# Performance work log

Hardware: AMD Instinct MI355X
Metric: run time of the kernel (lower is better)

Reference implementation:

```python
import jax, jax.numpy as jnp
import numpy as np

EPS = 1e-5

def conv(x, w, groups=1):
    # x: NCHW, w: OIHW, VALID padding, stride 1 (cross-correlation, same as torch conv2d)
    return jax.lax.conv_general_dilated(x, w, (1, 1), 'VALID',
                                        feature_group_count=groups,
                                        dimension_numbers=('NCHW', 'OIHW', 'NCHW'))

def bn(x, g, b, m, v):
    # eval-mode batchnorm with running stats
    scale = (g / jnp.sqrt(v + EPS))[None, :, None, None]
    return (x - m[None, :, None, None]) * scale + b[None, :, None, None]

def xcorr_depthwise(x, k):
    # x: [B,C,Hs,Ws] search, k: [B,C,Hk,Wk] per-sample kernels
    B, C, H, W = x.shape
    xr = x.reshape(1, B * C, H, W)
    kr = k.reshape(B * C, 1, k.shape[2], k.shape[3])
    out = conv(xr, kr, groups=B * C)  # [1, B*C, Ho, Wo]
    return out.reshape(B, C, out.shape[2], out.shape[3])

def setup_inputs() -> dict:
    key = jax.random.key(0)
    ks = jax.random.split(key, 16)
    Cin, Hid, Cout = 256, 256, 20
    inp = {
        'kernel': jax.random.normal(ks[0], (128, Cin, 7, 7), jnp.float32),
        'search': jax.random.normal(ks[1], (128, Cin, 31, 31), jnp.float32),
        'wk': jax.random.normal(ks[2], (Hid, Cin, 3, 3), jnp.float32) * 0.02,
        'gk': jnp.ones((Hid,), jnp.float32),
        'bk': jnp.zeros((Hid,), jnp.float32),
        'mk': jax.random.normal(ks[3], (Hid,), jnp.float32) * 0.1,
        'vk': jax.random.uniform(ks[4], (Hid,), jnp.float32) + 0.5,
        'ws': jax.random.normal(ks[5], (Hid, Cin, 3, 3), jnp.float32) * 0.02,
        'gs': jnp.ones((Hid,), jnp.float32),
        'bs': jnp.zeros((Hid,), jnp.float32),
        'ms': jax.random.normal(ks[6], (Hid,), jnp.float32) * 0.1,
        'vs': jax.random.uniform(ks[7], (Hid,), jnp.float32) + 0.5,
        'wh1': jax.random.normal(ks[8], (Hid, Hid, 1, 1), jnp.float32) * 0.02,
        'gh': jnp.ones((Hid,), jnp.float32),
        'bh': jnp.zeros((Hid,), jnp.float32),
        'mh': jax.random.normal(ks[9], (Hid,), jnp.float32) * 0.1,
        'vh': jax.random.uniform(ks[10], (Hid,), jnp.float32) + 0.5,
        'wh2': jax.random.normal(ks[11], (Cout, Hid, 1, 1), jnp.float32) * 0.02,
        'bh2': jnp.zeros((Cout,), jnp.float32),
    }
    return inp

def reference(kernel, search, wk, gk, bk, mk, vk, ws, gs, bs, ms, vs,
              wh1, gh, bh, mh, vh, wh2, bh2):
    k = jax.nn.relu(bn(conv(kernel, wk), gk, bk, mk, vk))   # [B,256,5,5]
    s = jax.nn.relu(bn(conv(search, ws), gs, bs, ms, vs))   # [B,256,29,29]
    f = xcorr_depthwise(s, k)                               # [B,256,25,25]
    h = jax.nn.relu(bn(conv(f, wh1), gh, bh, mh, vh))
    out = conv(h, wh2) + bh2[None, :, None, None]           # [B,20,25,25]
    return out
```

## Files before the change

kernel.cpp:

```cpp
#include <hip/hip_runtime.h>

typedef __bf16 bf16x8 __attribute__((ext_vector_type(8)));
typedef float floatx4 __attribute__((ext_vector_type(4)));
typedef unsigned short u16;
typedef unsigned int u32;

__device__ __forceinline__ u16 f2bf(float f) {
    union { float f; unsigned int u; } q; q.f = f;
    unsigned int r = q.u + 0x7FFFu + ((q.u >> 16) & 1u);
    return (u16)(r >> 16);
}
__device__ __forceinline__ float bf2f(u16 b) {
    union { unsigned int u; float f; } q; q.u = ((unsigned int)b) << 16;
    return q.f;
}

__device__ __forceinline__ void gl2lds16(const u16* g, u16* l) {
    __builtin_amdgcn_global_load_lds((const __attribute__((address_space(1))) u32*)g,
                                     (__attribute__((address_space(3))) u32*)l, 16, 0, 0);
}

__global__ __launch_bounds__(256) void prep_and_transpose(
    const float* __restrict__ kin, u16* __restrict__ KIN,
    const float* __restrict__ sin_, u16* __restrict__ SIN,
    const float* __restrict__ wk, const float* __restrict__ wsw, const float* __restrict__ wh1,
    const float* __restrict__ gk, const float* __restrict__ bk,
    const float* __restrict__ mk, const float* __restrict__ vk,
    const float* __restrict__ gs, const float* __restrict__ bs,
    const float* __restrict__ ms, const float* __restrict__ vs,
    const float* __restrict__ gh, const float* __restrict__ bh,
    const float* __restrict__ mh, const float* __restrict__ vh,
    u16* __restrict__ WKP, u16* __restrict__ WSP, u16* __restrict__ WH1P,
    float* __restrict__ par)
{
    __shared__ float tile[64][33];
    int bid = blockIdx.x, t = threadIdx.x;
    if (bid < 16896) {
        const float* in; u16* out; int HW, sptiles;
        if (bid < 1024) { in = kin;  out = KIN; HW = 49;  sptiles = 2; }
        else { bid -= 1024; in = sin_; out = SIN; HW = 961; sptiles = 31; }
        int st  = bid % sptiles;
        int tmp = bid / sptiles;
        int ct  = tmp & 3;
        int b   = tmp >> 2;
        int sp0 = st * 32, ci0 = ct * 64;
        int j = t & 31, i8 = t >> 5;
        const float* ip = in + ((size_t)b * 256 + ci0 + i8) * HW + sp0 + j;
#pragma unroll
        for (int k = 0; k < 8; ++k) {
            if (sp0 + j < HW) tile[i8 + k * 8][j] = ip[(size_t)(k * 8) * HW];
        }
        __syncthreads();
        int cl = t & 63, s4 = t >> 6;
#pragma unroll
        for (int k = 0; k < 8; ++k) {
            int spl = s4 + k * 4;
            int sp  = sp0 + spl;
            if (sp < HW) out[((size_t)b * HW + sp) * 256 + ci0 + cl] = f2bf(tile[cl][spl]);
        }
        return;
    }
    bid -= 16896;
    if (bid < 4608) {
        const float* src = (bid < 2304) ? wk : wsw;
        u16* dst = (bid < 2304) ? WKP : WSP;
        int tid = ((bid < 2304) ? bid : bid - 2304) * 256 + t;
        int o  = tid / 2304;
        int k  = tid - o * 2304;
        int rc = k >> 8;
        int ci = k & 255;
        dst[tid] = f2bf(src[o * 2304 + ci * 9 + rc]);
    } else if (bid < 4864) {
        int tid = (bid - 4608) * 256 + t;
        WH1P[tid] = f2bf(wh1[tid]);
    } else {
        float s;
        s = gk[t] * rsqrtf(vk[t] + 1e-5f); par[0*256+t] = s; par[1*256+t] = bk[t] - mk[t]*s;
        s = gs[t] * rsqrtf(vs[t] + 1e-5f); par[2*256+t] = s; par[3*256+t] = bs[t] - ms[t]*s;
        s = gh[t] * rsqrtf(vh[t] + 1e-5f); par[4*256+t] = s; par[5*256+t] = bh[t] - mh[t]*s;
    }
}

__global__ __launch_bounds__(256) void conv_gemm(
    const u16* __restrict__ Ain, const u16* __restrict__ Wpk,
    const float* __restrict__ scale, const float* __restrict__ shift,
    u16* __restrict__ Out,
    int OHW, int OW, int IW, int bstride, int KW, int nrc, int mblocks)
{
    __shared__ u16 Alds[4096];
    __shared__ u16 Blds[4096];

    const int tot = mblocks * 2;
    const int grp = (tot >> 3) << 3;
    const int lid = blockIdx.x;
    const int nid = (lid < grp) ? ((lid & 7) * (grp >> 3) + (lid >> 3)) : lid;
    const int m0 = (nid >> 1) * 128;
    const int n0 = (nid & 1) * 128;

    const int t    = threadIdx.x;
    const int wave = t >> 6;
    const int lane = t & 63;
    const int quad = lane >> 4;
    const int lrow = lane & 15;

    const int koff = (((t & 3) ^ ((t >> 3) & 3)) << 3);
    const int r0 = t >> 2;
    int m_a0 = m0 + r0;
    int b0 = m_a0 / OHW; int rem0 = m_a0 - b0 * OHW; int y0 = rem0 / OW; int x0 = rem0 - y0 * OW;
    int m_a1 = m_a0 + 64;
    int b1 = m_a1 / OHW; int rem1 = m_a1 - b1 * OHW; int y1 = rem1 / OW; int x1 = rem1 - y1 * OW;
    const u16* ag0 = Ain + (size_t)b0 * bstride + (size_t)(y0 * IW + x0) * 256 + koff;
    const u16* ag1 = Ain + (size_t)b1 * bstride + (size_t)(y1 * IW + x1) * 256 + koff;
    const int Ktot = nrc * 256;
    const u16* bg0 = Wpk + (size_t)(n0 + r0) * Ktot + koff;
    const u16* bg1 = bg0 + (size_t)64 * Ktot;

    u16* lA0 = Alds + wave * 512;
    u16* lA1 = Alds + 2048 + wave * 512;
    u16* lB0 = Blds + wave * 512;
    u16* lB1 = Blds + 2048 + wave * 512;

    floatx4 zero = {0.f, 0.f, 0.f, 0.f};
    floatx4 acc[4][4];
#pragma unroll
    for (int i = 0; i < 4; ++i)
#pragma unroll
        for (int j = 0; j < 4; ++j) acc[i][j] = zero;

    const int wr  = (wave >> 1) << 6;
    const int wc  = (wave & 1) << 6;
    const int pos = ((quad ^ ((lrow >> 1) & 3)) << 3);

    const int nchunks = nrc << 3;
    for (int ch = 0; ch < nchunks; ++ch) {
        int rc  = ch >> 3;
        int ci0 = (ch & 7) << 5;
        int rr  = rc / KW;
        int cc  = rc - rr * KW;
        int ao  = (rr * IW + cc) * 256 + ci0;
        int bo  = ch << 5;
        __syncthreads();
        gl2lds16(ag0 + ao, lA0);
        gl2lds16(ag1 + ao, lA1);
        gl2lds16(bg0 + bo, lB0);
        gl2lds16(bg1 + bo, lB1);
        __syncthreads();
        bf16x8 af[4], bfr[4];
#pragma unroll
        for (int mi = 0; mi < 4; ++mi)
            af[mi] = *(const bf16x8*)&Alds[(wr + mi * 16 + lrow) * 32 + pos];
#pragma unroll
        for (int ni = 0; ni < 4; ++ni)
            bfr[ni] = *(const bf16x8*)&Blds[(wc + ni * 16 + lrow) * 32 + pos];
#pragma unroll
        for (int mi = 0; mi < 4; ++mi)
#pragma unroll
            for (int ni = 0; ni < 4; ++ni)
                acc[mi][ni] = __builtin_amdgcn_mfma_f32_16x16x32_bf16(af[mi], bfr[ni], acc[mi][ni], 0, 0, 0);
    }

    float sc[4], sh[4];
#pragma unroll
    for (int ni = 0; ni < 4; ++ni) {
        int gn = n0 + wc + ni * 16 + lrow;
        sc[ni] = scale[gn];
        sh[ni] = shift[gn];
    }
#pragma unroll
    for (int mi = 0; mi < 4; ++mi) {
        int gm = m0 + wr + mi * 16 + (quad << 2);
#pragma unroll
        for (int ri = 0; ri < 4; ++ri) {
            size_t ro = (size_t)(gm + ri) * 256 + n0 + wc + lrow;
#pragma unroll
            for (int ni = 0; ni < 4; ++ni) {
                float v = acc[mi][ni][ri] * sc[ni] + sh[ni];
                v = fmaxf(v, 0.f);
                Out[ro + ni * 16] = f2bf(v);
            }
        }
    }
}

#define NS_BLK 421
__global__ __launch_bounds__(512, 2) void conv_gemm256(
    const u16* __restrict__ AinS, const u16* __restrict__ WpkS,
    const float* __restrict__ parS, u16* __restrict__ OutS,
    const u16* __restrict__ AinK, const u16* __restrict__ WpkK,
    const float* __restrict__ parK, u16* __restrict__ OutK)
{
    __shared__ __align__(16) u16 Alds[2][256][64];
    __shared__ __align__(16) u16 Blds[2][256][64];

    const int Ktot = 2304;
    const int NKT  = 36;
    const int KW   = 3;

    const int lid = blockIdx.x;
    const bool isk = (lid >= NS_BLK);

    int nid;
    if (!isk) {
        const int xcd = lid & 7, sub = lid >> 3;
        nid = (xcd < 5) ? (xcd * 53 + sub) : (265 + (xcd - 5) * 52 + sub);
    } else {
        nid = lid - NS_BLK;
    }
    const int m0 = nid << 8;

    const int OHW     = isk ? 25    : 841;
    const int OW      = isk ? 5     : 29;
    const int IW      = isk ? 7     : 31;
    const int bstride = isk ? 12544 : 246016;
    const int Mtot    = isk ? 3200  : 107648;
    const u16* Ain    = isk ? AinK : AinS;
    const u16* Wpk    = isk ? WpkK : WpkS;
    const float* scale = isk ? parK : parS;
    const float* shift = scale + 256;
    u16* Out          = isk ? OutK : OutS;

    const int t     = threadIdx.x;
    const int wave  = t >> 6;
    const int lane  = t & 63;
    const int lrow  = lane & 15;
    const int lquad = lane >> 4;
    const int wmBase = (wave >> 2) << 7;
    const int wnBase = (wave & 3) << 6;

    const u16* pA[4];
    const u16* pB[4];
#pragma unroll
    for (int j = 0; j < 4; ++j) {
        int u = j * 512 + t;
        int row = u >> 3, slot = u & 7;
        int ko = ((slot ^ (row & 7)) << 3);
        int m = m0 + row; if (m >= Mtot) m = Mtot - 1;
        int b = m / OHW; int rem = m - b * OHW; int y = rem / OW; int x = rem - y * OW;
        pA[j] = Ain + (size_t)b * bstride + (size_t)(y * IW + x) * 256 + ko;
        pB[j] = Wpk + (size_t)row * (size_t)Ktot + ko;
    }

    const int xo0 = ((lquad ^ (lrow & 7)) << 3);
    const int xo1 = xo0 ^ 32;

    floatx4 acc[8][4];
#pragma unroll
    for (int i = 0; i < 8; ++i)
#pragma unroll
        for (int j = 0; j < 4; ++j) acc[i][j] = (floatx4){0.f, 0.f, 0.f, 0.f};

#pragma unroll
    for (int j = 0; j < 4; ++j)
        gl2lds16(pA[j], &Alds[0][0][0] + j * 4096 + wave * 512);
#pragma unroll
    for (int j = 0; j < 4; ++j)
        gl2lds16(pB[j], &Blds[0][0][0] + j * 4096 + wave * 512);
    asm volatile("s_waitcnt vmcnt(0)" ::: "memory");
    __builtin_amdgcn_s_barrier();

#define LOADA(mb) do {                                              \
        const u16* _p = Ab + (wmBase + (mb) * 16 + lrow) * 64;      \
        aF[0][0] = *(const bf16x8*)(_p + xo0);                      \
        aF[0][1] = *(const bf16x8*)(_p + xo1);                      \
        aF[1][0] = *(const bf16x8*)(_p + 1024 + xo0);               \
        aF[1][1] = *(const bf16x8*)(_p + 1024 + xo1);               \
    } while (0)

#define MFMA16(mb) do {                                                                               \
        _Pragma("unroll")                                                                             \
        for (int _n = 0; _n < 4; ++_n) {                                                              \
            acc[(mb)][_n]     = __builtin_amdgcn_mfma_f32_16x16x32_bf16(aF[0][0], bB[_n][0], acc[(mb)][_n], 0, 0, 0);     \
            acc[(mb)][_n]     = __builtin_amdgcn_mfma_f32_16x16x32_bf16(aF[0][1], bB[_n][1], acc[(mb)][_n], 0, 0, 0);     \
            acc[(mb) + 1][_n] = __builtin_amdgcn_mfma_f32_16x16x32_bf16(aF[1][0], bB[_n][0], acc[(mb) + 1][_n], 0, 0, 0); \
            acc[(mb) + 1][_n] = __builtin_amdgcn_mfma_f32_16x16x32_bf16(aF[1][1], bB[_n][1], acc[(mb) + 1][_n], 0, 0, 0); \
        }                                                                                             \
    } while (0)

#pragma unroll 2
    for (int kt = 0; kt < NKT; ++kt) {
        const int c = kt & 1;
        const u16* Ab = &Alds[c][0][0];
        const u16* Bb = &Blds[c][0][0];
        u16* An = &Alds[c ^ 1][0][0];
        u16* Bn = &Blds[c ^ 1][0][0];
        const int pf = (kt + 1 < NKT);
        const int kt1 = kt + 1;
        const int rc = kt1 >> 2;
        const int rr = rc / KW;
        const int cc = rc - rr * KW;
        const int aoffA = (rr * IW + cc) * 256 + ((kt1 & 3) << 6);
        const int boffB = kt1 << 6;

        if (pf) {
#pragma unroll
            for (int j = 0; j < 4; ++j)
                gl2lds16(pA[j] + aoffA, An + j * 4096 + wave * 512);
#pragma unroll
            for (int j = 0; j < 4; ++j)
                gl2lds16(pB[j] + boffB, Bn + j * 4096 + wave * 512);
        }

        bf16x8 bB[4][2];
        bf16x8 aF[2][2];
#pragma unroll
        for (int ni = 0; ni < 4; ++ni) {
            const u16* _p = Bb + (wnBase + ni * 16 + lrow) * 64;
            bB[ni][0] = *(const bf16x8*)(_p + xo0);
            bB[ni][1] = *(const bf16x8*)(_p + xo1);
        }
        LOADA(0);
        MFMA16(0);
        LOADA(2);
        MFMA16(2);
        LOADA(4);
        MFMA16(4);
        LOADA(6);
        MFMA16(6);

        asm volatile("s_waitcnt vmcnt(0)" ::: "memory");
        __builtin_amdgcn_s_barrier();
    }

#undef LOADA
#undef MFMA16

    float sc[4], sh[4];
#pragma unroll
    for (int ni = 0; ni < 4; ++ni) {
        int gn = wnBase + ni * 16 + lrow;
        sc[ni] = scale[gn];
        sh[ni] = shift[gn];
    }
#pragma unroll
    for (int mi = 0; mi < 8; ++mi) {
        int gm0 = m0 + wmBase + mi * 16 + (lquad << 2);
#pragma unroll
        for (int ri = 0; ri < 4; ++ri) {
            int gm = gm0 + ri;
            if (gm < Mtot) {
                size_t ro = (size_t)gm * 256 + wnBase + lrow;
#pragma unroll
                for (int ni = 0; ni < 4; ++ni) {
                    float v = acc[mi][ni][ri] * sc[ni] + sh[ni];
                    v = fmaxf(v, 0.f);
                    Out[ro + ni * 16] = f2bf(v);
                }
            }
        }
    }
}

__global__ __launch_bounds__(256) void xcorr(const u16* __restrict__ ss, const u16* __restrict__ kk,
                                             u16* __restrict__ f) {
    __shared__ __align__(16) u16 Srow[29 * 256];

    int lid = blockIdx.x;
    int bid = (lid & 7) * 400 + (lid >> 3);
    int b = bid / 25, y = bid - b * 25;
    int t = threadIdx.x;
    int cg = (t & 31) << 3;
    int xg = t >> 5;
    const u16* kbase = kk + (size_t)b * 25 * 256 + cg;
    const u16* sbase = ss + (size_t)(b * 29 + y) * 29 * 256;

    float acc[4][8];
#pragma unroll
    for (int j = 0; j < 4; ++j)
#pragma unroll
        for (int e = 0; e < 8; ++e) acc[j][e] = 0.f;

#pragma unroll
    for (int r = 0; r < 5; ++r) {
        __syncthreads();
        const u16* grow = sbase + (size_t)r * 29 * 256;
        for (int i = t; i < 928; i += 256)
            *(bf16x8*)&Srow[i * 8] = *(const bf16x8*)&grow[i * 8];
        __syncthreads();
#pragma unroll
        for (int c = 0; c < 5; ++c) {
            bf16x8 kv = *(const bf16x8*)(kbase + (r * 5 + c) * 256);
            float kf[8];
#pragma unroll
            for (int e = 0; e < 8; ++e) kf[e] = (float)kv[e];
#pragma unroll
            for (int j = 0; j < 4; ++j) {
                int x = xg + 8 * j;
                if (x < 25) {
                    bf16x8 sv = *(const bf16x8*)&Srow[(x + c) * 256 + cg];
#pragma unroll
                    for (int e = 0; e < 8; ++e) acc[j][e] += (float)sv[e] * kf[e];
                }
            }
        }
    }

    u16* fb = f + (size_t)(b * 25 + y) * 25 * 256 + cg;
#pragma unroll
    for (int j = 0; j < 4; ++j) {
        int x = xg + 8 * j;
        if (x < 25) {
            u16 pk[8];
#pragma unroll
            for (int e = 0; e < 8; ++e) pk[e] = f2bf(acc[j][e]);
            *(bf16x8*)(fb + (size_t)x * 256) = *(const bf16x8*)pk;
        }
    }
}

__global__ __launch_bounds__(256) void head(const u16* __restrict__ h, const float* __restrict__ w2,
                                            const float* __restrict__ b2, float* __restrict__ out) {
    __shared__ __align__(16) u16   hl[25 * 264];
    __shared__ __align__(16) float wl[20 * 260];
    int bid = blockIdx.x;
    int b = bid / 25, y = bid - b * 25;
    int t = threadIdx.x;
    const u16* hrow = h + (size_t)(b * 25 + y) * 25 * 256;
    for (int i = t; i < 800; i += 256) {
        int x = i >> 5, c8 = i & 31;
        *(bf16x8*)&hl[x * 264 + c8 * 8] = *(const bf16x8*)&hrow[i * 8];
    }
    for (int i = t; i < 1280; i += 256) {
        int co = i >> 6, c4 = i & 63;
        *(float4*)&wl[co * 260 + c4 * 4] = *(const float4*)&w2[(size_t)co * 256 + c4 * 4];
    }
    __syncthreads();
    for (int o = t; o < 500; o += 256) {
        int x = o / 20, co = o - x * 20;
        float acc = b2[co];
        const u16* hp = &hl[x * 264];
        const float* wp = &wl[co * 260];
#pragma unroll 4
        for (int k = 0; k < 256; k += 8) {
            bf16x8 hv = *(const bf16x8*)(hp + k);
            float4 w0 = *(const float4*)(wp + k);
            float4 w1v = *(const float4*)(wp + k + 4);
            acc += (float)hv[0] * w0.x + (float)hv[1] * w0.y
                 + (float)hv[2] * w0.z + (float)hv[3] * w0.w
                 + (float)hv[4] * w1v.x + (float)hv[5] * w1v.y
                 + (float)hv[6] * w1v.z + (float)hv[7] * w1v.w;
        }
        out[(size_t)((b * 20 + co) * 25 + y) * 25 + x] = acc;
    }
}

#define OFF_SIN  0ull
#define SZ_SIN   62980096ull
#define OFF_KIN  (OFF_SIN + SZ_SIN)
#define SZ_KIN   3211264ull
#define OFF_WKP  (OFF_KIN + SZ_KIN)
#define SZ_WKP   1179648ull
#define OFF_WSP  (OFF_WKP + SZ_WKP)
#define SZ_WSP   1179648ull
#define OFF_WH1P (OFF_WSP + SZ_WSP)
#define SZ_WH1P  131072ull
#define OFF_PAR  (OFF_WH1P + SZ_WH1P)
#define SZ_PAR   8192ull
#define OFF_KK   (OFF_PAR + SZ_PAR)
#define SZ_KK    1638400ull
#define OFF_SS   (OFF_KK + SZ_KK)
#define SZ_SS    55115776ull
#define OFF_F    OFF_SIN
#define OFF_H    OFF_SS

extern "C" void kernel_launch(void* const* d_in, const int* in_sizes, int n_in,
                              void* d_out, int out_size, void* d_ws, size_t ws_size,
                              hipStream_t stream) {
    const float* kin  = (const float*)d_in[0];
    const float* sin_ = (const float*)d_in[1];
    const float* wk   = (const float*)d_in[2];
    const float* gk   = (const float*)d_in[3];
    const float* bk   = (const float*)d_in[4];
    const float* mk   = (const float*)d_in[5];
    const float* vk   = (const float*)d_in[6];
    const float* wsw  = (const float*)d_in[7];
    const float* gs   = (const float*)d_in[8];
    const float* bs   = (const float*)d_in[9];
    const float* ms   = (const float*)d_in[10];
    const float* vs   = (const float*)d_in[11];
    const float* wh1  = (const float*)d_in[12];
    const float* gh   = (const float*)d_in[13];
    const float* bh   = (const float*)d_in[14];
    const float* mh   = (const float*)d_in[15];
    const float* vh   = (const float*)d_in[16];
    const float* wh2  = (const float*)d_in[17];
    const float* bh2  = (const float*)d_in[18];
    float* out = (float*)d_out;

    char* w = (char*)d_ws;
    u16*   SIN  = (u16*)(w + OFF_SIN);
    u16*   KIN  = (u16*)(w + OFF_KIN);
    u16*   WKP  = (u16*)(w + OFF_WKP);
    u16*   WSP  = (u16*)(w + OFF_WSP);
    u16*   WH1P = (u16*)(w + OFF_WH1P);
    float* PAR  = (float*)(w + OFF_PAR);
    u16*   KK   = (u16*)(w + OFF_KK);
    u16*   SS   = (u16*)(w + OFF_SS);
    u16*   F    = (u16*)(w + OFF_F);
    u16*   H    = (u16*)(w + OFF_H);

    prep_and_transpose<<<21761, 256, 0, stream>>>(kin, KIN, sin_, SIN,
                                                  wk, wsw, wh1,
                                                  gk, bk, mk, vk, gs, bs, ms, vs, gh, bh, mh, vh,
                                                  WKP, WSP, WH1P, PAR);

    conv_gemm256<<<434, 512, 0, stream>>>(SIN, WSP, PAR + 512, SS,
                                          KIN, WKP, PAR + 0, KK);
    xcorr<<<3200, 256, 0, stream>>>(SS, KK, F);
    conv_gemm<<<1250, 256, 0, stream>>>(F, WH1P, PAR + 1024, PAR + 1280, H,
                                        625, 25, 25, 160000, 1, 1, 625);
    head<<<3200, 256, 0, stream>>>(H, wh2, bh2, out);

    (void)in_sizes; (void)n_in; (void)out_size; (void)ws_size;
}
```

Measured before the change: 461.5 us.

## Replace 1x1 head conv GEMM with 256x256-tile double-buffered kernel

Swaps the generic 128x128-tile conv_gemm used for the 1x1 hidden conv for a dedicated 512-thread kernel. Each block covers 256 rows and all 256 output channels, using 64-wide K tiles that are double-buffered in LDS with async global-to-LDS prefetch. The goal is to cut the number of LDS barriers and global reloads of F and the weights, and to overlap loads with MFMA work. In exchange it uses more LDS and registers per block, and only 313 blocks run, which may leave some CUs underused.

```diff
diff --git a/kernel.cpp b/kernel.cpp
--- a/kernel.cpp
+++ b/kernel.cpp
@@ -81,107 +81,6 @@
     }
 }
 
-__global__ __launch_bounds__(256) void conv_gemm(
-    const u16* __restrict__ Ain, const u16* __restrict__ Wpk,
-    const float* __restrict__ scale, const float* __restrict__ shift,
-    u16* __restrict__ Out,
-    int OHW, int OW, int IW, int bstride, int KW, int nrc, int mblocks)
-{
-    __shared__ u16 Alds[4096];
-    __shared__ u16 Blds[4096];
-
-    const int tot = mblocks * 2;
-    const int grp = (tot >> 3) << 3;
-    const int lid = blockIdx.x;
-    const int nid = (lid < grp) ? ((lid & 7) * (grp >> 3) + (lid >> 3)) : lid;
-    const int m0 = (nid >> 1) * 128;
-    const int n0 = (nid & 1) * 128;
-
-    const int t    = threadIdx.x;
-    const int wave = t >> 6;
-    const int lane = t & 63;
-    const int quad = lane >> 4;
-    const int lrow = lane & 15;
-
-    const int koff = (((t & 3) ^ ((t >> 3) & 3)) << 3);
-    const int r0 = t >> 2;
-    int m_a0 = m0 + r0;
-    int b0 = m_a0 / OHW; int rem0 = m_a0 - b0 * OHW; int y0 = rem0 / OW; int x0 = rem0 - y0 * OW;
-    int m_a1 = m_a0 + 64;
-    int b1 = m_a1 / OHW; int rem1 = m_a1 - b1 * OHW; int y1 = rem1 / OW; int x1 = rem1 - y1 * OW;
-    const u16* ag0 = Ain + (size_t)b0 * bstride + (size_t)(y0 * IW + x0) * 256 + koff;
-    const u16* ag1 = Ain + (size_t)b1 * bstride + (size_t)(y1 * IW + x1) * 256 + koff;
-    const int Ktot = nrc * 256;
-    const u16* bg0 = Wpk + (size_t)(n0 + r0) * Ktot + koff;
-    const u16* bg1 = bg0 + (size_t)64 * Ktot;
-
-    u16* lA0 = Alds + wave * 512;
-    u16* lA1 = Alds + 2048 + wave * 512;
-    u16* lB0 = Blds + wave * 512;
-    u16* lB1 = Blds + 2048 + wave * 512;
-
-    floatx4 zero = {0.f, 0.f, 0.f, 0.f};
-    floatx4 acc[4][4];
-#pragma unroll
-    for (int i = 0; i < 4; ++i)
-#pragma unroll
-        for (int j = 0; j < 4; ++j) acc[i][j] = zero;
-
-    const int wr  = (wave >> 1) << 6;
-    const int wc  = (wave & 1) << 6;
-    const int pos = ((quad ^ ((lrow >> 1) & 3)) << 3);
-
-    const int nchunks = nrc << 3;
-    for (int ch = 0; ch < nchunks; ++ch) {
-        int rc  = ch >> 3;
-        int ci0 = (ch & 7) << 5;
-        int rr  = rc / KW;
-        int cc  = rc - rr * KW;
-        int ao  = (rr * IW + cc) * 256 + ci0;
-        int bo  = ch << 5;
-        __syncthreads();
-        gl2lds16(ag0 + ao, lA0);
-        gl2lds16(ag1 + ao, lA1);
-        gl2lds16(bg0 + bo, lB0);
-        gl2lds16(bg1 + bo, lB1);
-        __syncthreads();
-        bf16x8 af[4], bfr[4];
-#pragma unroll
-        for (int mi = 0; mi < 4; ++mi)
-            af[mi] = *(const bf16x8*)&Alds[(wr + mi * 16 + lrow) * 32 + pos];
-#pragma unroll
-        for (int ni = 0; ni < 4; ++ni)
-            bfr[ni] = *(const bf16x8*)&Blds[(wc + ni * 16 + lrow) * 32 + pos];
-#pragma unroll
-        for (int mi = 0; mi < 4; ++mi)
-#pragma unroll
-            for (int ni = 0; ni < 4; ++ni)
-                acc[mi][ni] = __builtin_amdgcn_mfma_f32_16x16x32_bf16(af[mi], bfr[ni], acc[mi][ni], 0, 0, 0);
-    }
-
-    float sc[4], sh[4];
-#pragma unroll
-    for (int ni = 0; ni < 4; ++ni) {
-        int gn = n0 + wc + ni * 16 + lrow;
-        sc[ni] = scale[gn];
-        sh[ni] = shift[gn];
-    }
-#pragma unroll
-    for (int mi = 0; mi < 4; ++mi) {
-        int gm = m0 + wr + mi * 16 + (quad << 2);
-#pragma unroll
-        for (int ri = 0; ri < 4; ++ri) {
-            size_t ro = (size_t)(gm + ri) * 256 + n0 + wc + lrow;
-#pragma unroll
-            for (int ni = 0; ni < 4; ++ni) {
-                float v = acc[mi][ni][ri] * sc[ni] + sh[ni];
-                v = fmaxf(v, 0.f);
-                Out[ro + ni * 16] = f2bf(v);
-            }
-        }
-    }
-}
-
 #define NS_BLK 421
 __global__ __launch_bounds__(512, 2) void conv_gemm256(
     const u16* __restrict__ AinS, const u16* __restrict__ WpkS,
@@ -344,6 +243,143 @@
                     float v = acc[mi][ni][ri] * sc[ni] + sh[ni];
                     v = fmaxf(v, 0.f);
                     Out[ro + ni * 16] = f2bf(v);
+                }
+            }
+        }
+    }
+}
+
+__global__ __launch_bounds__(512, 2) void conv1x1_g256(
+    const u16* __restrict__ F, const u16* __restrict__ W1,
+    const float* __restrict__ par, u16* __restrict__ H)
+{
+    __shared__ __align__(16) u16 Alds[2][256][64];
+    __shared__ __align__(16) u16 Blds[2][256][64];
+
+    const int NKT  = 4;
+    const int Mtot = 80000;
+
+    const int m0 = blockIdx.x << 8;
+
+    const int t     = threadIdx.x;
+    const int wave  = t >> 6;
+    const int lane  = t & 63;
+    const int lrow  = lane & 15;
+    const int lquad = lane >> 4;
+    const int wmBase = (wave >> 2) << 7;
+    const int wnBase = (wave & 3) << 6;
+
+    const u16* pA[4];
+    const u16* pB[4];
+#pragma unroll
+    for (int j = 0; j < 4; ++j) {
+        int u = j * 512 + t;
+        int row = u >> 3, slot = u & 7;
+        int ko = ((slot ^ (row & 7)) << 3);
+        int m = m0 + row; if (m >= Mtot) m = Mtot - 1;
+        pA[j] = F  + (size_t)m * 256 + ko;
+        pB[j] = W1 + (size_t)row * 256 + ko;
+    }
+
+    const int xo0 = ((lquad ^ (lrow & 7)) << 3);
+    const int xo1 = xo0 ^ 32;
+
+    floatx4 acc[8][4];
+#pragma unroll
+    for (int i = 0; i < 8; ++i)
+#pragma unroll
+        for (int j = 0; j < 4; ++j) acc[i][j] = (floatx4){0.f, 0.f, 0.f, 0.f};
+
+#pragma unroll
+    for (int j = 0; j < 4; ++j)
+        gl2lds16(pA[j], &Alds[0][0][0] + j * 4096 + wave * 512);
+#pragma unroll
+    for (int j = 0; j < 4; ++j)
+        gl2lds16(pB[j], &Blds[0][0][0] + j * 4096 + wave * 512);
+    asm volatile("s_waitcnt vmcnt(0)" ::: "memory");
+    __builtin_amdgcn_s_barrier();
+
+#define LOADA(mb) do {                                              \
+        const u16* _p = Ab + (wmBase + (mb) * 16 + lrow) * 64;      \
+        aF[0][0] = *(const bf16x8*)(_p + xo0);                      \
+        aF[0][1] = *(const bf16x8*)(_p + xo1);                      \
+        aF[1][0] = *(const bf16x8*)(_p + 1024 + xo0);               \
+        aF[1][1] = *(const bf16x8*)(_p + 1024 + xo1);               \
+    } while (0)
+
+#define MFMA16(mb) do {                                                                               \
+        _Pragma("unroll")                                                                             \
+        for (int _n = 0; _n < 4; ++_n) {                                                              \
+            acc[(mb)][_n]     = __builtin_amdgcn_mfma_f32_16x16x32_bf16(aF[0][0], bB[_n][0], acc[(mb)][_n], 0, 0, 0);     \
+            acc[(mb)][_n]     = __builtin_amdgcn_mfma_f32_16x16x32_bf16(aF[0][1], bB[_n][1], acc[(mb)][_n], 0, 0, 0);     \
+            acc[(mb) + 1][_n] = __builtin_amdgcn_mfma_f32_16x16x32_bf16(aF[1][0], bB[_n][0], acc[(mb) + 1][_n], 0, 0, 0); \
+            acc[(mb) + 1][_n] = __builtin_amdgcn_mfma_f32_16x16x32_bf16(aF[1][1], bB[_n][1], acc[(mb) + 1][_n], 0, 0, 0); \
+        }                                                                                             \
+    } while (0)
+
+#pragma unroll
+    for (int kt = 0; kt < NKT; ++kt) {
+        const int c = kt & 1;
+        const u16* Ab = &Alds[c][0][0];
+        const u16* Bb = &Blds[c][0][0];
+        u16* An = &Alds[c ^ 1][0][0];
+        u16* Bn = &Blds[c ^ 1][0][0];
+        const int pf = (kt + 1 < NKT);
+        const int koff = (kt + 1) << 6;
+
+        if (pf) {
+#pragma unroll
+            for (int j = 0; j < 4; ++j)
+                gl2lds16(pA[j] + koff, An + j * 4096 + wave * 512);
+#pragma unroll
+            for (int j = 0; j < 4; ++j)
+                gl2lds16(pB[j] + koff, Bn + j * 4096 + wave * 512);
+        }
+
+        bf16x8 bB[4][2];
+        bf16x8 aF[2][2];
+#pragma unroll
+        for (int ni = 0; ni < 4; ++ni) {
+            const u16* _p = Bb + (wnBase + ni * 16 + lrow) * 64;
+            bB[ni][0] = *(const bf16x8*)(_p + xo0);
+            bB[ni][1] = *(const bf16x8*)(_p + xo1);
+        }
+        LOADA(0);
+        MFMA16(0);
+        LOADA(2);
+        MFMA16(2);
+        LOADA(4);
+        MFMA16(4);
+        LOADA(6);
+        MFMA16(6);
+
+        asm volatile("s_waitcnt vmcnt(0)" ::: "memory");
+        __builtin_amdgcn_s_barrier();
+    }
+
+#undef LOADA
+#undef MFMA16
+
+    float sc[4], sh[4];
+#pragma unroll
+    for (int ni = 0; ni < 4; ++ni) {
+        int gn = wnBase + ni * 16 + lrow;
+        sc[ni] = par[gn];
+        sh[ni] = par[256 + gn];
+    }
+#pragma unroll
+    for (int mi = 0; mi < 8; ++mi) {
+        int gm0 = m0 + wmBase + mi * 16 + (lquad << 2);
+#pragma unroll
+        for (int ri = 0; ri < 4; ++ri) {
+            int gm = gm0 + ri;
+            if (gm < Mtot) {
+                size_t ro = (size_t)gm * 256 + wnBase + lrow;
+#pragma unroll
+                for (int ni = 0; ni < 4; ++ni) {
+                    float v = acc[mi][ni][ri] * sc[ni] + sh[ni];
+                    v = fmaxf(v, 0.f);
+                    H[ro + ni * 16] = f2bf(v);
                 }
             }
         }
@@ -506,8 +542,7 @@
     conv_gemm256<<<434, 512, 0, stream>>>(SIN, WSP, PAR + 512, SS,
                                           KIN, WKP, PAR + 0, KK);
     xcorr<<<3200, 256, 0, stream>>>(SS, KK, F);
-    conv_gemm<<<1250, 256, 0, stream>>>(F, WH1P, PAR + 1024, PAR + 1280, H,
-                                        625, 25, 25, 160000, 1, 1, 625);
+    conv1x1_g256<<<313, 512, 0, stream>>>(F, WH1P, PAR + 1024, H);
     head<<<3200, 256, 0, stream>>>(H, wh2, bh2, out);
 
     (void)in_sizes; (void)n_in; (void)out_size; (void)ws_size;
```

After: 475.0 us. 2.9% more time.
